# Optimization experiments

Measured on AMD Instinct MI355X. Metric: run time of the kernel, lower is better.

Reference implementation:

```python
import jax, jax.numpy as jnp
import numpy as np

B, D, G, H = 65536, 512, 16, 128


def setup_inputs() -> dict:
    key = jax.random.key(0)
    ks = jax.random.split(key, 8)
    s = 1.0 / np.sqrt(D)
    sh = 1.0 / np.sqrt(H)
    return {
        "z": jax.random.normal(ks[0], (B, D), dtype=jnp.float32),
        "Wc": jax.random.uniform(ks[1], (D, G), jnp.float32, -s, s),
        "bc": jax.random.uniform(ks[2], (G,), jnp.float32, -s, s),
        "W1": jax.random.uniform(ks[3], (G, D, H), jnp.float32, -s, s),
        "b1": jax.random.uniform(ks[4], (G, H), jnp.float32, -s, s),
        "W2": jax.random.uniform(ks[5], (G, H), jnp.float32, -sh, sh),
        "b2": jax.random.uniform(ks[6], (G,), jnp.float32, -sh, sh),
    }


def reference(z, Wc, bc, W1, b1, W2, b2):
    # classifier head + softmax
    logits = z @ Wc + bc                                  # [B, G]
    p_g = jax.nn.softmax(logits, axis=1)                  # [B, G]
    # G experts fused as one batched GEMM: fc1 -> GELU -> fc2 (dropout = identity at eval)
    h = jax.nn.gelu(jnp.einsum('bd,gdh->bgh', z, W1) + b1, approximate=False)  # [B, G, H]
    y_all = jnp.einsum('bgh,gh->bg', h, W2) + b2          # [B, G]
    return logits, p_g, y_all
```

## Files before the change

### kernel.cpp

```cpp
#include <hip/hip_runtime.h>
#include <cstdint>
#include <cstddef>

typedef __bf16 bf16x8 __attribute__((ext_vector_type(8)));
typedef float f32x4 __attribute__((ext_vector_type(4)));
typedef unsigned short ushortx8 __attribute__((ext_vector_type(8)));

__device__ __forceinline__ unsigned short f2bf(float f) {
  union { float f; unsigned int u; } v; v.f = f;
  return (unsigned short)((v.u + 0x8000u) >> 16);
}

__device__ __forceinline__ float gelu_s(float x) {
  float x2 = x * x;
  float p = __builtin_fmaf(x2, -0.10294324f, -2.30220819f);
  float e = __builtin_amdgcn_exp2f(x * p);
  return x * __builtin_amdgcn_rcpf(1.0f + e);
}

#define GLOAD16(gsrc, ldst)                                                  \
  __builtin_amdgcn_global_load_lds(                                          \
      (const __attribute__((address_space(1))) unsigned int*)(gsrc),         \
      (__attribute__((address_space(3))) unsigned int*)(uintptr_t)(          \
          (char*)(ldst)),                                                    \
      16, 0, 0)

#define SWZ_FRAG(base, R, C8)                                                \
  (*(const bf16x8*)((base) + (((R) >> 5) * 4096) +                           \
                    ((((R)&31) * 8 + ((C8) ^ ((R)&7))) * 16)))

__global__ __launch_bounds__(256) void k_convert(
    const float* __restrict__ z, const float* __restrict__ W1,
    const float* __restrict__ Wc, unsigned short* __restrict__ zb,
    unsigned short* __restrict__ w1t, unsigned short* __restrict__ wct) {
  int bid = blockIdx.x;
  int tid = threadIdx.x;
  if (bid < 16384) {
    size_t i = ((size_t)bid * 256 + tid) * 8;
    const float4* p = (const float4*)(z + i);
    float4 a = p[0], b = p[1];
    ushortx8 r;
    r[0] = f2bf(a.x); r[1] = f2bf(a.y); r[2] = f2bf(a.z); r[3] = f2bf(a.w);
    r[4] = f2bf(b.x); r[5] = f2bf(b.y); r[6] = f2bf(b.z); r[7] = f2bf(b.w);
    *(ushortx8*)(zb + i) = r;
  } else if (bid < 16384 + 1024) {
    __shared__ float tile[32][33];
    int b = bid - 16384;
    int gg = b >> 6;
    int t = b & 63;
    int d0 = (t >> 2) * 32;
    int h0 = (t & 3) * 32;
    int tx = tid & 31, ty = tid >> 5;
#pragma unroll
    for (int r = 0; r < 4; ++r) {
      int d = d0 + r * 8 + ty;
      tile[r * 8 + ty][tx] = W1[(gg << 16) + d * 128 + h0 + tx];
    }
    __syncthreads();
#pragma unroll
    for (int r = 0; r < 4; ++r) {
      int h = h0 + r * 8 + ty;
      w1t[(gg << 16) + h * 512 + d0 + tx] = f2bf(tile[tx][r * 8 + ty]);
    }
  } else {
#pragma unroll
    for (int j = 0; j < 32; ++j) {
      int i = j * 256 + tid;
      wct[(i & 15) * 512 + (i >> 4)] = f2bf(Wc[i]);
    }
  }
}

__global__ __launch_bounds__(256, 3) void k_main(
    const unsigned short* __restrict__ zb,
    const unsigned short* __restrict__ w1t,
    const unsigned short* __restrict__ wct,
    const float* __restrict__ bc, const float* __restrict__ b1,
    const float* __restrict__ w2, const float* __restrict__ b2,
    float* __restrict__ out) {
  __shared__ alignas(16) char lds[8192 + 32768 + 1024];
  const int tid = threadIdx.x;
  const int wq = tid >> 6;
  const int ln = tid & 63;
  const int l15 = ln & 15;
  const int l4 = ln >> 4;
  const int c8s = (((tid & 7) ^ ((tid >> 3) & 7))) * 8;
  char* ldsB = lds + 8192;

  if (blockIdx.x >= 512) {
    const int eb = blockIdx.x - 512;
    const int p = eb >> 10;
    const int mbase = (eb & 1023) * 64;
    const unsigned short* ag = zb + (size_t)(mbase + (tid >> 3)) * 512 + c8s;
    const unsigned short* bg = w1t + p * 131072 + (tid >> 3) * 512 + c8s;
    const int e = p * 2 + (wq >> 1);
    const int nb = (wq & 1) * 64;
    f32x4 acc[4][4] = {};
    for (int kt = 0; kt < 8; ++kt) {
      const int ko = kt * 64;
#pragma unroll
      for (int it = 0; it < 2; ++it)
        GLOAD16(ag + it * 32 * 512 + ko, lds + it * 4096 + tid * 16);
#pragma unroll
      for (int it = 0; it < 8; ++it)
        GLOAD16(bg + it * 32 * 512 + ko, ldsB + it * 4096 + tid * 16);
      __syncthreads();
#pragma unroll
      for (int ks = 0; ks < 2; ++ks) {
        bf16x8 af[4];
#pragma unroll
        for (int rt = 0; rt < 4; ++rt)
          af[rt] = SWZ_FRAG(lds, rt * 16 + l15, ks * 4 + l4);
#pragma unroll
        for (int ct = 0; ct < 4; ++ct) {
          bf16x8 bf = SWZ_FRAG(ldsB, wq * 64 + ct * 16 + l15, ks * 4 + l4);
#pragma unroll
          for (int rt = 0; rt < 4; ++rt)
            acc[rt][ct] = __builtin_amdgcn_mfma_f32_16x16x32_bf16(
                af[rt], bf, acc[rt][ct], 0, 0, 0);
        }
      }
      __syncthreads();
    }
    float b1v[4], w2v[4];
#pragma unroll
    for (int ct = 0; ct < 4; ++ct) {
      int n = nb + ct * 16 + l15;
      b1v[ct] = b1[e * 128 + n];
      w2v[ct] = w2[e * 128 + n];
    }
    float* ylds = (float*)(lds + 40960);
#pragma unroll
    for (int rt = 0; rt < 4; ++rt) {
#pragma unroll
      for (int i = 0; i < 4; ++i) {
        float s = 0.0f;
#pragma unroll
        for (int ct = 0; ct < 4; ++ct)
          s += gelu_s(acc[rt][ct][i] + b1v[ct]) * w2v[ct];
#pragma unroll
        for (int off = 1; off < 16; off <<= 1)
          s += __shfl_xor(s, off, 16);
        if (l15 == 0) ylds[wq * 64 + rt * 16 + l4 * 4 + i] = s;
      }
    }
    __syncthreads();
    if (tid < 128) {
      int row = tid & 63, ee = tid >> 6;
      float y = ylds[ee * 128 + row] + ylds[ee * 128 + 64 + row] +
                b2[p * 2 + ee];
      out[(size_t)2097152 + (size_t)(mbase + row) * 16 + p * 2 + ee] = y;
    }
  } else {
    const int mbase = blockIdx.x * 128;
    const unsigned short* ag = zb + (size_t)(mbase + (tid >> 3)) * 512 + c8s;
    const unsigned short* wb = wct + l15 * 512 + l4 * 8;
    f32x4 acc2[2] = {};
    for (int kt = 0; kt < 8; ++kt) {
      const int ko = kt * 64;
#pragma unroll
      for (int it = 0; it < 4; ++it)
        GLOAD16(ag + it * 32 * 512 + ko, lds + it * 4096 + tid * 16);
      bf16x8 bfr0 = *(const bf16x8*)(wb + ko);
      bf16x8 bfr1 = *(const bf16x8*)(wb + ko + 32);
      __syncthreads();
#pragma unroll
      for (int rt = 0; rt < 2; ++rt) {
        bf16x8 a0 = SWZ_FRAG(lds, wq * 32 + rt * 16 + l15, l4);
        acc2[rt] = __builtin_amdgcn_mfma_f32_16x16x32_bf16(a0, bfr0, acc2[rt],
                                                           0, 0, 0);
        bf16x8 a1 = SWZ_FRAG(lds, wq * 32 + rt * 16 + l15, 4 + l4);
        acc2[rt] = __builtin_amdgcn_mfma_f32_16x16x32_bf16(a1, bfr1, acc2[rt],
                                                           0, 0, 0);
      }
      __syncthreads();
    }
    float bcv = bc[l15];
#pragma unroll
    for (int rt = 0; rt < 2; ++rt) {
#pragma unroll
      for (int i = 0; i < 4; ++i) {
        int row = wq * 32 + rt * 16 + l4 * 4 + i;
        float lg = acc2[rt][i] + bcv;
        float mx = lg;
#pragma unroll
        for (int off = 1; off < 16; off <<= 1)
          mx = fmaxf(mx, __shfl_xor(mx, off, 16));
        float ex = __expf(lg - mx);
        float sm = ex;
#pragma unroll
        for (int off = 1; off < 16; off <<= 1)
          sm += __shfl_xor(sm, off, 16);
        size_t ro = (size_t)(mbase + row) * 16 + l15;
        out[ro] = lg;
        out[1048576 + ro] = ex / sm;
      }
    }
  }
}

extern "C" void kernel_launch(void* const* d_in, const int* in_sizes, int n_in,
                              void* d_out, int out_size, void* d_ws,
                              size_t ws_size, hipStream_t stream) {
  const float* z = (const float*)d_in[0];
  const float* Wc = (const float*)d_in[1];
  const float* bc = (const float*)d_in[2];
  const float* W1 = (const float*)d_in[3];
  const float* b1 = (const float*)d_in[4];
  const float* W2 = (const float*)d_in[5];
  const float* b2 = (const float*)d_in[6];
  float* out = (float*)d_out;

  unsigned short* zb = (unsigned short*)d_ws;
  unsigned short* w1t = zb + (size_t)65536 * 512;
  unsigned short* wct = w1t + (size_t)16 * 128 * 512;

  k_convert<<<16384 + 1024 + 1, 256, 0, stream>>>(z, W1, Wc, zb, w1t, wct);
  k_main<<<512 + 8 * 1024, 256, 0, stream>>>(zb, w1t, wct, bc, b1, W2, b2,
                                             out);
}
```

Baseline: 401.4 us.

## Split logits into own kernel and keep expert weights register-resident in main GEMM

The classifier/softmax path moves out of the combined kernel into its own k_logits launch. The expert kernel now gives each block one expert and 1024 rows. The expert's full W1 slice is held in registers as bf16 fragments and reused across 16 row tiles, using 32x32x16 MFMAs. K is split across wave pairs, whose partial sums are combined through LDS before GELU and the W2 reduction. This removes repeated reloading of W1 tiles from memory, at the cost of very high register pressure, an extra kernel launch, and more LDS syncs per tile.

```diff
diff --git a/kernel.cpp b/kernel.cpp
--- a/kernel.cpp
+++ b/kernel.cpp
@@ -4,6 +4,7 @@
 
 typedef __bf16 bf16x8 __attribute__((ext_vector_type(8)));
 typedef float f32x4 __attribute__((ext_vector_type(4)));
+typedef float f32x16 __attribute__((ext_vector_type(16)));
 typedef unsigned short ushortx8 __attribute__((ext_vector_type(8)));
 
 __device__ __forceinline__ unsigned short f2bf(float f) {
@@ -71,131 +72,184 @@
   }
 }
 
-__global__ __launch_bounds__(256, 3) void k_main(
+__global__ __launch_bounds__(256) void k_logits(
     const unsigned short* __restrict__ zb,
-    const unsigned short* __restrict__ w1t,
-    const unsigned short* __restrict__ wct,
-    const float* __restrict__ bc, const float* __restrict__ b1,
-    const float* __restrict__ w2, const float* __restrict__ b2,
+    const unsigned short* __restrict__ wct, const float* __restrict__ bc,
     float* __restrict__ out) {
-  __shared__ alignas(16) char lds[8192 + 32768 + 1024];
+  __shared__ alignas(16) char lds[16384];
   const int tid = threadIdx.x;
   const int wq = tid >> 6;
   const int ln = tid & 63;
   const int l15 = ln & 15;
   const int l4 = ln >> 4;
   const int c8s = (((tid & 7) ^ ((tid >> 3) & 7))) * 8;
-  char* ldsB = lds + 8192;
-
-  if (blockIdx.x >= 512) {
-    const int eb = blockIdx.x - 512;
-    const int p = eb >> 10;
-    const int mbase = (eb & 1023) * 64;
-    const unsigned short* ag = zb + (size_t)(mbase + (tid >> 3)) * 512 + c8s;
-    const unsigned short* bg = w1t + p * 131072 + (tid >> 3) * 512 + c8s;
-    const int e = p * 2 + (wq >> 1);
-    const int nb = (wq & 1) * 64;
-    f32x4 acc[4][4] = {};
-    for (int kt = 0; kt < 8; ++kt) {
-      const int ko = kt * 64;
-#pragma unroll
-      for (int it = 0; it < 2; ++it)
-        GLOAD16(ag + it * 32 * 512 + ko, lds + it * 4096 + tid * 16);
-#pragma unroll
-      for (int it = 0; it < 8; ++it)
-        GLOAD16(bg + it * 32 * 512 + ko, ldsB + it * 4096 + tid * 16);
-      __syncthreads();
-#pragma unroll
-      for (int ks = 0; ks < 2; ++ks) {
-        bf16x8 af[4];
-#pragma unroll
-        for (int rt = 0; rt < 4; ++rt)
-          af[rt] = SWZ_FRAG(lds, rt * 16 + l15, ks * 4 + l4);
-#pragma unroll
-        for (int ct = 0; ct < 4; ++ct) {
-          bf16x8 bf = SWZ_FRAG(ldsB, wq * 64 + ct * 16 + l15, ks * 4 + l4);
-#pragma unroll
-          for (int rt = 0; rt < 4; ++rt)
-            acc[rt][ct] = __builtin_amdgcn_mfma_f32_16x16x32_bf16(
-                af[rt], bf, acc[rt][ct], 0, 0, 0);
+  const int mbase = blockIdx.x * 128;
+  const unsigned short* ag = zb + (size_t)(mbase + (tid >> 3)) * 512 + c8s;
+  const unsigned short* wb = wct + l15 * 512 + l4 * 8;
+  f32x4 acc2[2] = {};
+  for (int kt = 0; kt < 8; ++kt) {
+    const int ko = kt * 64;
+#pragma unroll
+    for (int it = 0; it < 4; ++it)
+      GLOAD16(ag + it * 32 * 512 + ko, lds + it * 4096 + tid * 16);
+    bf16x8 bfr0 = *(const bf16x8*)(wb + ko);
+    bf16x8 bfr1 = *(const bf16x8*)(wb + ko + 32);
+    __syncthreads();
+#pragma unroll
+    for (int rt = 0; rt < 2; ++rt) {
+      bf16x8 a0 = SWZ_FRAG(lds, wq * 32 + rt * 16 + l15, l4);
+      acc2[rt] =
+          __builtin_amdgcn_mfma_f32_16x16x32_bf16(a0, bfr0, acc2[rt], 0, 0, 0);
+      bf16x8 a1 = SWZ_FRAG(lds, wq * 32 + rt * 16 + l15, 4 + l4);
+      acc2[rt] =
+          __builtin_amdgcn_mfma_f32_16x16x32_bf16(a1, bfr1, acc2[rt], 0, 0, 0);
+    }
+    __syncthreads();
+  }
+  float bcv = bc[l15];
+#pragma unroll
+  for (int rt = 0; rt < 2; ++rt) {
+#pragma unroll
+    for (int i = 0; i < 4; ++i) {
+      int row = wq * 32 + rt * 16 + l4 * 4 + i;
+      float lg = acc2[rt][i] + bcv;
+      float mx = lg;
+#pragma unroll
+      for (int off = 1; off < 16; off <<= 1)
+        mx = fmaxf(mx, __shfl_xor(mx, off, 16));
+      float ex = __expf(lg - mx);
+      float sm = ex;
+#pragma unroll
+      for (int off = 1; off < 16; off <<= 1)
+        sm += __shfl_xor(sm, off, 16);
+      size_t ro = (size_t)(mbase + row) * 16 + l15;
+      out[ro] = lg;
+      out[1048576 + ro] = ex / sm;
+    }
+  }
+}
+
+__global__ __launch_bounds__(256, 2) void k_main(
+    const unsigned short* __restrict__ zb,
+    const unsigned short* __restrict__ w1t,
+    const float* __restrict__ b1, const float* __restrict__ w2,
+    const float* __restrict__ b2, float* __restrict__ out) {
+  __shared__ alignas(16) char lds[65536];
+  const int tid = threadIdx.x;
+  const int wv = tid >> 6;
+  const int ln = tid & 63;
+  const int l31 = ln & 31;
+  const int l5 = ln >> 5;
+  const int kh = wv >> 1;
+  const int ch = wv & 1;
+  const int e = blockIdx.x & 15;
+  const int mg = blockIdx.x >> 4;
+  const size_t m0g = (size_t)mg * 1024;
+
+  bf16x8 bfr[2][16];
+  {
+    const unsigned short* bp =
+        w1t + e * 65536 + (ch * 64 + l31) * 512 + kh * 256 + l5 * 8;
+#pragma unroll
+    for (int ct = 0; ct < 2; ++ct)
+#pragma unroll
+      for (int ks = 0; ks < 16; ++ks)
+        bfr[ct][ks] = *(const bf16x8*)(bp + ct * 16384 + ks * 16);
+  }
+  const int col = ch * 64 + kh * 32 + l31;
+  const float b1v = b1[e * 128 + col];
+  const float w2v = w2[e * 128 + col];
+  const float b2v = b2[e];
+
+  const int Ce = (tid & 63) ^ wv;
+  const unsigned short* agE = zb + (m0g + wv) * 512 + Ce * 8;
+  const unsigned short* agO = zb + (m0g + wv) * 512 + (Ce ^ 4) * 8;
+
+  int abase[4];
+#pragma unroll
+  for (int j = 0; j < 4; ++j)
+    abase[j] = l31 * 1024 + kh * 512 + (((j * 2 + l5) ^ (l31 & 7)) * 16);
+
+  const int cs = ch * 32 + l31;
+  const int csx = cs & 7;
+
+  for (int it = 0; it < 16; ++it) {
+    f32x16 acc[2][2] = {};
+#pragma unroll
+    for (int it2 = 0; it2 < 16; ++it2) {
+      const unsigned short* src =
+          ((it2 & 1) ? agO : agE) + (it * 64 + it2 * 4) * 512;
+      GLOAD16(src, lds + it2 * 4096 + tid * 16);
+    }
+    __syncthreads();
+#pragma unroll
+    for (int ks = 0; ks < 16; ++ks) {
+      const int ao = abase[ks & 3] + (ks >> 2) * 128;
+      bf16x8 af0 = *(const bf16x8*)(lds + ao);
+      bf16x8 af1 = *(const bf16x8*)(lds + ao + 32768);
+      acc[0][0] = __builtin_amdgcn_mfma_f32_32x32x16_bf16(af0, bfr[0][ks],
+                                                          acc[0][0], 0, 0, 0);
+      acc[0][1] = __builtin_amdgcn_mfma_f32_32x32x16_bf16(af0, bfr[1][ks],
+                                                          acc[0][1], 0, 0, 0);
+      acc[1][0] = __builtin_amdgcn_mfma_f32_32x32x16_bf16(af1, bfr[0][ks],
+                                                          acc[1][0], 0, 0, 0);
+      acc[1][1] = __builtin_amdgcn_mfma_f32_32x32x16_bf16(af1, bfr[1][ks],
+                                                          acc[1][1], 0, 0, 0);
+    }
+    __syncthreads();
+    {
+      char* reg = lds + (kh ? 0 : 16384);
+      const int donate = kh ^ 1;
+#pragma unroll
+      for (int rt = 0; rt < 2; ++rt)
+#pragma unroll
+        for (int q = 0; q < 4; ++q) {
+          int chunk = rt * 8 + q * 2 + l5;
+          f32x4 v;
+#pragma unroll
+          for (int i = 0; i < 4; ++i) v[i] = acc[rt][donate][q * 4 + i];
+          *(f32x4*)(reg + cs * 256 + ((chunk ^ csx) * 16)) = v;
+        }
+    }
+    __syncthreads();
+    {
+      char* reg = lds + (kh ? 16384 : 0);
+      float* yp = (float*)(lds + 32768);
+#pragma unroll
+      for (int rt = 0; rt < 2; ++rt) {
+        float s[16];
+#pragma unroll
+        for (int q = 0; q < 4; ++q) {
+          int chunk = rt * 8 + q * 2 + l5;
+          f32x4 v = *(const f32x4*)(reg + cs * 256 + ((chunk ^ csx) * 16));
+#pragma unroll
+          for (int i = 0; i < 4; ++i) {
+            float h = acc[rt][kh][q * 4 + i] + v[i] + b1v;
+            s[q * 4 + i] = gelu_s(h) * w2v;
+          }
+        }
+#pragma unroll
+        for (int off = 1; off < 32; off <<= 1)
+#pragma unroll
+          for (int j = 0; j < 16; ++j) s[j] += __shfl_xor(s[j], off, 64);
+        if (l31 == 0) {
+#pragma unroll
+          for (int q = 0; q < 4; ++q) {
+            f32x4 v;
+#pragma unroll
+            for (int i = 0; i < 4; ++i) v[i] = s[q * 4 + i];
+            *(f32x4*)(yp + wv * 64 + rt * 32 + q * 8 + l5 * 4) = v;
+          }
         }
       }
-      __syncthreads();
-    }
-    float b1v[4], w2v[4];
-#pragma unroll
-    for (int ct = 0; ct < 4; ++ct) {
-      int n = nb + ct * 16 + l15;
-      b1v[ct] = b1[e * 128 + n];
-      w2v[ct] = w2[e * 128 + n];
-    }
-    float* ylds = (float*)(lds + 40960);
-#pragma unroll
-    for (int rt = 0; rt < 4; ++rt) {
-#pragma unroll
-      for (int i = 0; i < 4; ++i) {
-        float s = 0.0f;
-#pragma unroll
-        for (int ct = 0; ct < 4; ++ct)
-          s += gelu_s(acc[rt][ct][i] + b1v[ct]) * w2v[ct];
-#pragma unroll
-        for (int off = 1; off < 16; off <<= 1)
-          s += __shfl_xor(s, off, 16);
-        if (l15 == 0) ylds[wq * 64 + rt * 16 + l4 * 4 + i] = s;
-      }
-    }
-    __syncthreads();
-    if (tid < 128) {
-      int row = tid & 63, ee = tid >> 6;
-      float y = ylds[ee * 128 + row] + ylds[ee * 128 + 64 + row] +
-                b2[p * 2 + ee];
-      out[(size_t)2097152 + (size_t)(mbase + row) * 16 + p * 2 + ee] = y;
-    }
-  } else {
-    const int mbase = blockIdx.x * 128;
-    const unsigned short* ag = zb + (size_t)(mbase + (tid >> 3)) * 512 + c8s;
-    const unsigned short* wb = wct + l15 * 512 + l4 * 8;
-    f32x4 acc2[2] = {};
-    for (int kt = 0; kt < 8; ++kt) {
-      const int ko = kt * 64;
-#pragma unroll
-      for (int it = 0; it < 4; ++it)
-        GLOAD16(ag + it * 32 * 512 + ko, lds + it * 4096 + tid * 16);
-      bf16x8 bfr0 = *(const bf16x8*)(wb + ko);
-      bf16x8 bfr1 = *(const bf16x8*)(wb + ko + 32);
-      __syncthreads();
-#pragma unroll
-      for (int rt = 0; rt < 2; ++rt) {
-        bf16x8 a0 = SWZ_FRAG(lds, wq * 32 + rt * 16 + l15, l4);
-        acc2[rt] = __builtin_amdgcn_mfma_f32_16x16x32_bf16(a0, bfr0, acc2[rt],
-                                                           0, 0, 0);
-        bf16x8 a1 = SWZ_FRAG(lds, wq * 32 + rt * 16 + l15, 4 + l4);
-        acc2[rt] = __builtin_amdgcn_mfma_f32_16x16x32_bf16(a1, bfr1, acc2[rt],
-                                                           0, 0, 0);
-      }
-      __syncthreads();
-    }
-    float bcv = bc[l15];
-#pragma unroll
-    for (int rt = 0; rt < 2; ++rt) {
-#pragma unroll
-      for (int i = 0; i < 4; ++i) {
-        int row = wq * 32 + rt * 16 + l4 * 4 + i;
-        float lg = acc2[rt][i] + bcv;
-        float mx = lg;
-#pragma unroll
-        for (int off = 1; off < 16; off <<= 1)
-          mx = fmaxf(mx, __shfl_xor(mx, off, 16));
-        float ex = __expf(lg - mx);
-        float sm = ex;
-#pragma unroll
-        for (int off = 1; off < 16; off <<= 1)
-          sm += __shfl_xor(sm, off, 16);
-        size_t ro = (size_t)(mbase + row) * 16 + l15;
-        out[ro] = lg;
-        out[1048576 + ro] = ex / sm;
-      }
-    }
+    }
+    __syncthreads();
+    if (wv == 0) {
+      const float* yp = (const float*)(lds + 32768);
+      float y = yp[ln] + yp[64 + ln] + yp[128 + ln] + yp[192 + ln] + b2v;
+      out[(size_t)2097152 + (m0g + it * 64 + ln) * 16 + e] = y;
+    }
+    __syncthreads();
   }
 }
 
@@ -216,6 +270,6 @@
   unsigned short* wct = w1t + (size_t)16 * 128 * 512;
 
   k_convert<<<16384 + 1024 + 1, 256, 0, stream>>>(z, W1, Wc, zb, w1t, wct);
-  k_main<<<512 + 8 * 1024, 256, 0, stream>>>(zb, w1t, wct, bc, b1, W2, b2,
-                                             out);
-}
+  k_logits<<<512, 256, 0, stream>>>(zb, wct, bc, out);
+  k_main<<<1024, 256, 0, stream>>>(zb, w1t, b1, W2, b2, out);
+}
```

After: 850.8 us. 112% more time.

## Split logits and expert kernels; enlarge expert tile to 128x256 with 8 waves

Applied to the files above, without the earlier changes.

Splits the combined kernel into a separate logits/softmax kernel and an expert GEMM kernel. The expert kernel now uses 512-thread blocks, each computing a 128-row by 256-column tile (two experts) instead of 64 rows. This halves the number of W1 tile reloads per row and doubles arithmetic intensity per LDS load. It also removes the branch divergence between block types. The cost is an extra kernel launch, higher LDS use per block, and possibly lower occupancy.

```diff
diff --git a/kernel.cpp b/kernel.cpp
--- a/kernel.cpp
+++ b/kernel.cpp
@@ -71,131 +71,140 @@
   }
 }
 
-__global__ __launch_bounds__(256, 3) void k_main(
+__global__ __launch_bounds__(256) void k_logits(
     const unsigned short* __restrict__ zb,
-    const unsigned short* __restrict__ w1t,
-    const unsigned short* __restrict__ wct,
-    const float* __restrict__ bc, const float* __restrict__ b1,
-    const float* __restrict__ w2, const float* __restrict__ b2,
+    const unsigned short* __restrict__ wct, const float* __restrict__ bc,
     float* __restrict__ out) {
-  __shared__ alignas(16) char lds[8192 + 32768 + 1024];
+  __shared__ alignas(16) char lds[16384];
   const int tid = threadIdx.x;
   const int wq = tid >> 6;
   const int ln = tid & 63;
   const int l15 = ln & 15;
   const int l4 = ln >> 4;
   const int c8s = (((tid & 7) ^ ((tid >> 3) & 7))) * 8;
-  char* ldsB = lds + 8192;
-
-  if (blockIdx.x >= 512) {
-    const int eb = blockIdx.x - 512;
-    const int p = eb >> 10;
-    const int mbase = (eb & 1023) * 64;
-    const unsigned short* ag = zb + (size_t)(mbase + (tid >> 3)) * 512 + c8s;
-    const unsigned short* bg = w1t + p * 131072 + (tid >> 3) * 512 + c8s;
-    const int e = p * 2 + (wq >> 1);
-    const int nb = (wq & 1) * 64;
-    f32x4 acc[4][4] = {};
-    for (int kt = 0; kt < 8; ++kt) {
-      const int ko = kt * 64;
-#pragma unroll
-      for (int it = 0; it < 2; ++it)
-        GLOAD16(ag + it * 32 * 512 + ko, lds + it * 4096 + tid * 16);
-#pragma unroll
-      for (int it = 0; it < 8; ++it)
-        GLOAD16(bg + it * 32 * 512 + ko, ldsB + it * 4096 + tid * 16);
-      __syncthreads();
-#pragma unroll
-      for (int ks = 0; ks < 2; ++ks) {
-        bf16x8 af[4];
+  const int mbase = blockIdx.x * 128;
+  const unsigned short* ag = zb + (size_t)(mbase + (tid >> 3)) * 512 + c8s;
+  const unsigned short* wb = wct + l15 * 512 + l4 * 8;
+  f32x4 acc2[2] = {};
+  for (int kt = 0; kt < 8; ++kt) {
+    const int ko = kt * 64;
+#pragma unroll
+    for (int it = 0; it < 4; ++it)
+      GLOAD16(ag + it * 32 * 512 + ko, lds + it * 4096 + tid * 16);
+    bf16x8 bfr0 = *(const bf16x8*)(wb + ko);
+    bf16x8 bfr1 = *(const bf16x8*)(wb + ko + 32);
+    __syncthreads();
+#pragma unroll
+    for (int rt = 0; rt < 2; ++rt) {
+      bf16x8 a0 = SWZ_FRAG(lds, wq * 32 + rt * 16 + l15, l4);
+      acc2[rt] =
+          __builtin_amdgcn_mfma_f32_16x16x32_bf16(a0, bfr0, acc2[rt], 0, 0, 0);
+      bf16x8 a1 = SWZ_FRAG(lds, wq * 32 + rt * 16 + l15, 4 + l4);
+      acc2[rt] =
+          __builtin_amdgcn_mfma_f32_16x16x32_bf16(a1, bfr1, acc2[rt], 0, 0, 0);
+    }
+    __syncthreads();
+  }
+  float bcv = bc[l15];
+#pragma unroll
+  for (int rt = 0; rt < 2; ++rt) {
+#pragma unroll
+    for (int i = 0; i < 4; ++i) {
+      int row = wq * 32 + rt * 16 + l4 * 4 + i;
+      float lg = acc2[rt][i] + bcv;
+      float mx = lg;
+#pragma unroll
+      for (int off = 1; off < 16; off <<= 1)
+        mx = fmaxf(mx, __shfl_xor(mx, off, 16));
+      float ex = __expf(lg - mx);
+      float sm = ex;
+#pragma unroll
+      for (int off = 1; off < 16; off <<= 1)
+        sm += __shfl_xor(sm, off, 16);
+      size_t ro = (size_t)(mbase + row) * 16 + l15;
+      out[ro] = lg;
+      out[1048576 + ro] = ex / sm;
+    }
+  }
+}
+
+__global__ __launch_bounds__(512, 6) void k_expert(
+    const unsigned short* __restrict__ zb,
+    const unsigned short* __restrict__ w1t,
+    const float* __restrict__ b1, const float* __restrict__ w2,
+    const float* __restrict__ b2, float* __restrict__ out) {
+  __shared__ alignas(16) char lds[16384 + 32768];
+  const int tid = threadIdx.x;
+  const int p = blockIdx.x & 7;
+  const int mbase = (blockIdx.x >> 3) * 128;
+  const int wv = tid >> 6;
+  const int ln = tid & 63;
+  const int l15 = ln & 15;
+  const int l4 = ln >> 4;
+  const int wr = wv & 1;
+  const int wc = wv >> 1;
+  const int e = p * 2 + (wc >> 1);
+  char* ldsB = lds + 16384;
+
+  const int c8s = (((tid & 7) ^ ((tid >> 3) & 7))) * 8;
+  const unsigned short* ag = zb + (size_t)(mbase + (tid >> 3)) * 512 + c8s;
+  const unsigned short* bg = w1t + p * 131072 + (tid >> 3) * 512 + c8s;
+
+  f32x4 acc[4][4] = {};
+  for (int kt = 0; kt < 8; ++kt) {
+    const int ko = kt * 64;
+#pragma unroll
+    for (int it = 0; it < 2; ++it)
+      GLOAD16(ag + it * 64 * 512 + ko, lds + it * 8192 + tid * 16);
+#pragma unroll
+    for (int it = 0; it < 4; ++it)
+      GLOAD16(bg + it * 64 * 512 + ko, ldsB + it * 8192 + tid * 16);
+    __syncthreads();
+#pragma unroll
+    for (int ks = 0; ks < 2; ++ks) {
+      bf16x8 af[4];
+#pragma unroll
+      for (int rt = 0; rt < 4; ++rt)
+        af[rt] = SWZ_FRAG(lds, wr * 64 + rt * 16 + l15, ks * 4 + l4);
+#pragma unroll
+      for (int ct = 0; ct < 4; ++ct) {
+        bf16x8 bf = SWZ_FRAG(ldsB, wc * 64 + ct * 16 + l15, ks * 4 + l4);
 #pragma unroll
         for (int rt = 0; rt < 4; ++rt)
-          af[rt] = SWZ_FRAG(lds, rt * 16 + l15, ks * 4 + l4);
-#pragma unroll
-        for (int ct = 0; ct < 4; ++ct) {
-          bf16x8 bf = SWZ_FRAG(ldsB, wq * 64 + ct * 16 + l15, ks * 4 + l4);
-#pragma unroll
-          for (int rt = 0; rt < 4; ++rt)
-            acc[rt][ct] = __builtin_amdgcn_mfma_f32_16x16x32_bf16(
-                af[rt], bf, acc[rt][ct], 0, 0, 0);
-        }
+          acc[rt][ct] = __builtin_amdgcn_mfma_f32_16x16x32_bf16(
+              af[rt], bf, acc[rt][ct], 0, 0, 0);
       }
-      __syncthreads();
-    }
-    float b1v[4], w2v[4];
-#pragma unroll
-    for (int ct = 0; ct < 4; ++ct) {
-      int n = nb + ct * 16 + l15;
-      b1v[ct] = b1[e * 128 + n];
-      w2v[ct] = w2[e * 128 + n];
-    }
-    float* ylds = (float*)(lds + 40960);
-#pragma unroll
-    for (int rt = 0; rt < 4; ++rt) {
-#pragma unroll
-      for (int i = 0; i < 4; ++i) {
-        float s = 0.0f;
-#pragma unroll
-        for (int ct = 0; ct < 4; ++ct)
-          s += gelu_s(acc[rt][ct][i] + b1v[ct]) * w2v[ct];
-#pragma unroll
-        for (int off = 1; off < 16; off <<= 1)
-          s += __shfl_xor(s, off, 16);
-        if (l15 == 0) ylds[wq * 64 + rt * 16 + l4 * 4 + i] = s;
-      }
-    }
-    __syncthreads();
-    if (tid < 128) {
-      int row = tid & 63, ee = tid >> 6;
-      float y = ylds[ee * 128 + row] + ylds[ee * 128 + 64 + row] +
-                b2[p * 2 + ee];
-      out[(size_t)2097152 + (size_t)(mbase + row) * 16 + p * 2 + ee] = y;
-    }
-  } else {
-    const int mbase = blockIdx.x * 128;
-    const unsigned short* ag = zb + (size_t)(mbase + (tid >> 3)) * 512 + c8s;
-    const unsigned short* wb = wct + l15 * 512 + l4 * 8;
-    f32x4 acc2[2] = {};
-    for (int kt = 0; kt < 8; ++kt) {
-      const int ko = kt * 64;
-#pragma unroll
-      for (int it = 0; it < 4; ++it)
-        GLOAD16(ag + it * 32 * 512 + ko, lds + it * 4096 + tid * 16);
-      bf16x8 bfr0 = *(const bf16x8*)(wb + ko);
-      bf16x8 bfr1 = *(const bf16x8*)(wb + ko + 32);
-      __syncthreads();
-#pragma unroll
-      for (int rt = 0; rt < 2; ++rt) {
-        bf16x8 a0 = SWZ_FRAG(lds, wq * 32 + rt * 16 + l15, l4);
-        acc2[rt] = __builtin_amdgcn_mfma_f32_16x16x32_bf16(a0, bfr0, acc2[rt],
-                                                           0, 0, 0);
-        bf16x8 a1 = SWZ_FRAG(lds, wq * 32 + rt * 16 + l15, 4 + l4);
-        acc2[rt] = __builtin_amdgcn_mfma_f32_16x16x32_bf16(a1, bfr1, acc2[rt],
-                                                           0, 0, 0);
-      }
-      __syncthreads();
-    }
-    float bcv = bc[l15];
-#pragma unroll
-    for (int rt = 0; rt < 2; ++rt) {
-#pragma unroll
-      for (int i = 0; i < 4; ++i) {
-        int row = wq * 32 + rt * 16 + l4 * 4 + i;
-        float lg = acc2[rt][i] + bcv;
-        float mx = lg;
-#pragma unroll
-        for (int off = 1; off < 16; off <<= 1)
-          mx = fmaxf(mx, __shfl_xor(mx, off, 16));
-        float ex = __expf(lg - mx);
-        float sm = ex;
-#pragma unroll
-        for (int off = 1; off < 16; off <<= 1)
-          sm += __shfl_xor(sm, off, 16);
-        size_t ro = (size_t)(mbase + row) * 16 + l15;
-        out[ro] = lg;
-        out[1048576 + ro] = ex / sm;
-      }
-    }
+    }
+    __syncthreads();
+  }
+  float b1v[4], w2v[4];
+#pragma unroll
+  for (int ct = 0; ct < 4; ++ct) {
+    int n = (wc & 1) * 64 + ct * 16 + l15;
+    b1v[ct] = b1[e * 128 + n];
+    w2v[ct] = w2[e * 128 + n];
+  }
+  float* ylds = (float*)lds;
+#pragma unroll
+  for (int rt = 0; rt < 4; ++rt) {
+#pragma unroll
+    for (int i = 0; i < 4; ++i) {
+      float s = 0.0f;
+#pragma unroll
+      for (int ct = 0; ct < 4; ++ct)
+        s += gelu_s(acc[rt][ct][i] + b1v[ct]) * w2v[ct];
+#pragma unroll
+      for (int off = 1; off < 16; off <<= 1)
+        s += __shfl_xor(s, off, 16);
+      if (l15 == 0) ylds[wc * 128 + wr * 64 + rt * 16 + l4 * 4 + i] = s;
+    }
+  }
+  __syncthreads();
+  if (tid < 256) {
+    int row = tid & 127, ei = tid >> 7;
+    float y = ylds[ei * 256 + row] + ylds[ei * 256 + 128 + row] +
+              b2[p * 2 + ei];
+    out[(size_t)2097152 + (size_t)(mbase + row) * 16 + p * 2 + ei] = y;
   }
 }
 
@@ -216,6 +225,6 @@
   unsigned short* wct = w1t + (size_t)16 * 128 * 512;
 
   k_convert<<<16384 + 1024 + 1, 256, 0, stream>>>(z, W1, Wc, zb, w1t, wct);
-  k_main<<<512 + 8 * 1024, 256, 0, stream>>>(zb, w1t, wct, bc, b1, W2, b2,
-                                             out);
-}
+  k_logits<<<512, 256, 0, stream>>>(zb, wct, bc, out);
+  k_expert<<<512 * 8, 512, 0, stream>>>(zb, w1t, b1, W2, b2, out);
+}
```

Result: slower. 1.048 ms (+161.0%).
